# Kernel tuning notes

Hardware: AMD Instinct MI355X
Metric: run time of the kernel (lower is better)

## Reference

```python
import jax, jax.numpy as jnp
import numpy as np

B, G, N_IN, N_HID, N_OUT = 2, 4096, 8, 32, 32
ALPHA, BETA, BN_EPS = 0.005, 5e-5, 1e-5
EDGE_P = 0.05  # adjacency density


def _lin_init(k, fan_in, fan_out):
    k1, k2 = jax.random.split(k)
    lim = 1.0 / np.sqrt(fan_in)
    W = jax.random.uniform(k1, (fan_in, fan_out), minval=-lim, maxval=lim, dtype=jnp.float32)
    b = jax.random.uniform(k2, (fan_out,), minval=-lim, maxval=lim, dtype=jnp.float32)
    return W, b


def setup_inputs() -> dict:
    key = jax.random.key(0)
    ks = jax.random.split(key, 12)
    W_infer, b_infer = _lin_init(ks[0], N_IN, N_HID)
    W_e1, b_e1 = _lin_init(ks[1], 2 * N_HID, 1)
    W_e2, b_e2 = _lin_init(ks[2], 2 * N_HID, 1)
    W_n1, b_n1 = _lin_init(ks[3], 2 * N_HID, N_OUT)
    W_n2, b_n2 = _lin_init(ks[4], 2 * N_HID, N_OUT)
    W_m1, b_m1 = _lin_init(ks[5], 2 * N_HID, N_OUT)
    W_m2, b_m2 = _lin_init(ks[6], 2 * N_HID, N_OUT)
    x = jax.random.normal(ks[7], (B, G, N_IN), dtype=jnp.float32)
    edges1 = jax.random.bernoulli(ks[8], EDGE_P, (G, G)).astype(jnp.float32)
    edges2 = jax.random.bernoulli(ks[9], EDGE_P, (G, G)).astype(jnp.float32)
    bn_gamma = jnp.ones((G,), jnp.float32)
    bn_beta = jnp.zeros((G,), jnp.float32)
    return dict(x=x, edges1=edges1, edges2=edges2, W_infer=W_infer, b_infer=b_infer,
                W_e1=W_e1, b_e1=b_e1, W_e2=W_e2, b_e2=b_e2,
                W_n1=W_n1, b_n1=b_n1, W_n2=W_n2, b_n2=b_n2,
                W_m1=W_m1, b_m1=b_m1, W_m2=W_m2, b_m2=b_m2,
                bn_gamma=bn_gamma, bn_beta=bn_beta)


def _mp_block(x, adj, coef, W_e, b_e, W_n, b_n, W_m, b_m):
    # x: [B,G,H]. Torch builds edge feature at flat index k=i*G+j as cat([x_j, x_i])
    # (shape2 = col gather, shape1 = row gather). We keep the same math without
    # materializing the [B,G*G,2H] tensor.
    Hh = x.shape[-1]
    s_src = x @ W_e[:Hh]   # [B,G,1]  (x_j part of mlp_edge)
    s_dst = x @ W_e[Hh:]   # [B,G,1]  (x_i part of mlp_edge)
    logits = s_dst[:, :, None, 0] + s_src[:, None, :, 0] + b_e[0]   # [B,G,G] at (i,j)
    w = adj + coef * (adj == 0).astype(x.dtype)                     # ori_edge + coef*thres_edge
    e = jax.nn.sigmoid(logits) * w[None]                            # [B,G,G]
    # receive at node i: sum_j e_ij * [x_j, x_i]
    recv_src = jnp.einsum('bij,bjh->bih', e, x)                     # sum_j e_ij x_j
    recv_dst = x * jnp.sum(e, axis=2)[..., None]                    # x_i * sum_j e_ij
    recv = jnp.concatenate([recv_src, recv_dst], axis=-1)           # [B,G,2H]
    recv = jax.nn.elu(recv @ W_n + b_n)                             # nodes_mlp + elu
    upd = jnp.concatenate([recv, x], axis=-1) @ W_m + b_m           # mesg_merge (mode='cat')
    return jax.nn.elu(upd)


def _forward(x, edges1, edges2, W_infer, b_infer, W_e1, b_e1, W_e2, b_e2,
             W_n1, b_n1, W_n2, b_n2, W_m1, b_m1, W_m2, b_m2, bn_gamma, bn_beta):
    h = jax.nn.elu(x @ W_infer + b_infer)                           # infer + elu, [B,G,H]
    h = _mp_block(h, edges1, ALPHA, W_e1, b_e1, W_n1, b_n1, W_m1, b_m1)
    # BatchNorm1d(gene_num) on [B, G, n_out]: per-gene stats over (batch, feature)
    mu = jnp.mean(h, axis=(0, 2), keepdims=True)
    var = jnp.var(h, axis=(0, 2), keepdims=True)
    h = (h - mu) * jax.lax.rsqrt(var + BN_EPS)
    h = h * bn_gamma[None, :, None] + bn_beta[None, :, None]
    return _mp_block(h, edges2, BETA, W_e2, b_e2, W_n2, b_n2, W_m2, b_m2)


def reference(x, edges1, edges2, W_infer, b_infer, W_e1, b_e1, W_e2, b_e2,
              W_n1, b_n1, W_n2, b_n2, W_m1, b_m1, W_m2, b_m2, bn_gamma, bn_beta):
    return _forward(x, edges1, edges2, W_infer, b_infer, W_e1, b_e1, W_e2, b_e2,
                    W_n1, b_n1, W_n2, b_n2, W_m1, b_m1, W_m2, b_m2, bn_gamma, bn_beta)
```

## Files before the change

### kernel.cpp

```cpp
#include <hip/hip_runtime.h>

#define G 4096
#define BSZ 2
#define NIN 8
#define HID 32
#define NLOG2E (-1.4426950408889634f)

typedef __attribute__((ext_vector_type(8))) short short8;
typedef __attribute__((ext_vector_type(4))) float floatx4;
typedef unsigned short ushort_t;
typedef unsigned int uint_t;

__device__ __forceinline__ float elu1(float v) {
    return v > 0.f ? v : (__expf(v) - 1.f);
}
__device__ __forceinline__ ushort_t f2bf(float f) {
    unsigned u = __float_as_uint(f);
    u += 0x7fffu + ((u >> 16) & 1u);
    return (ushort_t)(u >> 16);
}

__global__ __launch_bounds__(256) void k_setup1(
    const float* __restrict__ x, const float* __restrict__ W,
    const float* __restrict__ bias, const float* __restrict__ We,
    float* __restrict__ h0, ushort_t* __restrict__ hTb,
    float* __restrict__ ssrc, float* __restrict__ sdst) {
    __shared__ __align__(16) ushort_t hs[HID][264];
    int tid = threadIdx.x;
    int t = blockIdx.x * 256 + tid;
    int b = t >> 12;
    int g0 = (blockIdx.x & 15) * 256;
    float xin[NIN];
    const float* xp = x + t * NIN;
#pragma unroll
    for (int k = 0; k < NIN; k++) xin[k] = xp[k];
    float ss = 0.f, sd = 0.f;
    float* hp = h0 + (size_t)t * HID;
#pragma unroll
    for (int o = 0; o < HID; o++) {
        float v = bias[o];
#pragma unroll
        for (int k = 0; k < NIN; k++) v += xin[k] * W[k * HID + o];
        v = elu1(v);
        hp[o] = v;
        hs[o][tid] = f2bf(v);
        ss += v * We[o];
        sd += v * We[HID + o];
    }
    ssrc[t] = ss;
    sdst[t] = sd;
    __syncthreads();
#pragma unroll
    for (int p = 0; p < 4; p++) {
        int row = p * 8 + (tid >> 5);
        int c = (tid & 31) * 8;
        short8 v8 = *(const short8*)&hs[row][c];
        *(short8*)(void*)&hTb[(size_t)(b * HID + row) * G + g0 + c] = v8;
    }
}

template <bool DO_BN>
__global__ __launch_bounds__(512, 2) void k_fused(
    const float* __restrict__ adj, const float* __restrict__ ssrc,
    const float* __restrict__ sdst, const ushort_t* __restrict__ hTb_in,
    const float* __restrict__ bep, float coef, const float* __restrict__ hin,
    const float* __restrict__ Wn, const float* __restrict__ bnb,
    const float* __restrict__ Wm, const float* __restrict__ bmb,
    const float* __restrict__ gamma, const float* __restrict__ beta,
    const float* __restrict__ We2, float* __restrict__ outp,
    ushort_t* __restrict__ hTb_out, float* __restrict__ s2s,
    float* __restrict__ s2d) {
    union SMemU {
        float ssm[BSZ][G];
        struct {
            float rec[32][68];
            float rec2[32][68];
            float esg[16][2];
            ushort_t tb[BSZ][HID][16];
        } p;
    };
    __shared__ __align__(16) SMemU sm;
    __shared__ __align__(16) uint_t abits[128][16];
    __shared__ __align__(16) float red[6][64][9];
    __shared__ __align__(16) float Wns[2048];
    __shared__ __align__(16) float Wms[2048];

    int tid = threadIdx.x;
    int g0 = blockIdx.x * 16;
    int l = tid & 63, w = tid >> 6;

    ((float4*)Wns)[tid] = ((const float4*)Wn)[tid];
    ((float4*)Wms)[tid] = ((const float4*)Wm)[tid];
#pragma unroll
    for (int r = 0; r < 4; r++) {
        int idx = r * 2048 + tid * 4;
        int bb = idx >> 12, j = idx & 4095;
        float4 s4 = *(const float4*)&ssrc[bb * G + j];
        s4.x *= NLOG2E; s4.y *= NLOG2E; s4.z *= NLOG2E; s4.w *= NLOG2E;
        *(float4*)&sm.ssm[bb][j] = s4;
    }
#pragma unroll
    for (int rr = 0; rr < 2; rr++) {
        int row = 2 * w + rr;
        const float* ar = adj + (size_t)(g0 + row) * G;
#pragma unroll
        for (int it = 0; it < 16; it++) {
            float4 v4 = *(const float4*)&ar[it * 256 + l * 4];
            uint_t nib = (uint_t)(v4.x != 0.f) | ((uint_t)(v4.y != 0.f) << 1) |
                         ((uint_t)(v4.z != 0.f) << 2) | ((uint_t)(v4.w != 0.f) << 3);
            uint_t wd = nib << ((l & 7) * 4);
            wd |= __shfl_xor(wd, 1);
            wd |= __shfl_xor(wd, 2);
            wd |= __shfl_xor(wd, 4);
            if ((l & 7) == 0) abits[it * 8 + (l >> 3)][row] = wd;
        }
    }

    int jq = w >> 1, b = w & 1;
    int m = l & 15, kg = l >> 4;
    float sd2 = (sdst[b * G + g0 + m] + bep[0]) * NLOG2E;
    float wm1 = 1.f - coef;
    int jstart = jq * 1024;
    const ushort_t* hb0 = hTb_in + (size_t)(b * HID + m) * G + jstart + kg * 8;
    const ushort_t* hb1 = hb0 + (size_t)16 * G;
    floatx4 c0 = {0.f, 0.f, 0.f, 0.f}, c1 = {0.f, 0.f, 0.f, 0.f};
    float es = 0.f;
    short8 pb0[2], pb1[2];
#pragma unroll
    for (int d = 0; d < 2; d++) {
        pb0[d] = *(const short8*)(const void*)(hb0 + d * 32);
        pb1[d] = *(const short8*)(const void*)(hb1 + d * 32);
    }
    __syncthreads();
    const float* svp = &sm.ssm[b][jstart + kg * 8];
    const uint_t* abp = &abits[jq * 32][m];

#pragma unroll 4
    for (int jc = 0; jc < 32; jc++) {
        int cur = jc & 1;
        short8 bf0 = pb0[cur], bf1 = pb1[cur];
        if (jc + 2 < 32) {
            int o = (jc + 2) * 32;
            pb0[cur] = *(const short8*)(const void*)(hb0 + o);
            pb1[cur] = *(const short8*)(const void*)(hb1 + o);
        }
        uint_t bw = abp[jc * 16];
        float4 s0 = *(const float4*)&svp[jc * 32];
        float4 s1 = *(const float4*)&svp[jc * 32 + 4];
        float sv[8] = {s0.x, s0.y, s0.z, s0.w, s1.x, s1.y, s1.z, s1.w};
        short8 af;
#pragma unroll
        for (int t = 0; t < 8; t++) {
            float bitf = (float)((bw >> (kg * 8 + t)) & 1u);
            float wgt = __builtin_fmaf(bitf, wm1, coef);
            float ex = exp2f(sd2 + sv[t]);
            float e = __builtin_amdgcn_rcpf(1.f + ex) * wgt;
            es += e;
            af[t] = (short)f2bf(e);
        }
        c0 = __builtin_amdgcn_mfma_f32_16x16x32_bf16(af, bf0, c0, 0, 0, 0);
        c1 = __builtin_amdgcn_mfma_f32_16x16x32_bf16(af, bf1, c1, 0, 0, 0);
    }
    if (jq) {
        int widx = (jq - 1) * 2 + b;
#pragma unroll
        for (int r = 0; r < 4; r++) {
            red[widx][l][r] = c0[r];
            red[widx][l][4 + r] = c1[r];
        }
        red[widx][l][8] = es;
    }
    __syncthreads();
    if (!jq) {
#pragma unroll
        for (int q = 0; q < 3; q++) {
            int widx = q * 2 + b;
#pragma unroll
            for (int r = 0; r < 4; r++) {
                c0[r] += red[widx][l][r];
                c1[r] += red[widx][l][4 + r];
            }
            es += red[widx][l][8];
        }
        es += __shfl_xor(es, 16);
        es += __shfl_xor(es, 32);
#pragma unroll
        for (int r = 0; r < 4; r++) {
            int gene = (l >> 4) * 4 + r;
            sm.p.rec[gene * 2 + b][m] = c0[r];
            sm.p.rec[gene * 2 + b][16 + m] = c1[r];
        }
        if (l < 16) sm.p.esg[l][b] = es;
    }
    __syncthreads();

    int rl = tid >> 5, hh = tid & 31;
#pragma unroll
    for (int rp = 0; rp < 2; rp++) {
        int row = rp * 16 + rl;
        int gene = row >> 1, bb = row & 1;
        float xv = hin[((size_t)(bb * G + g0 + gene)) * HID + hh];
        sm.p.rec[row][32 + hh] = xv * sm.p.esg[gene][bb];
    }
    __syncthreads();

#pragma unroll
    for (int rp = 0; rp < 2; rp++) {
        int row = rp * 16 + rl;
        int gene = row >> 1, bb = row & 1;
        float v = bnb[hh];
#pragma unroll
        for (int k4 = 0; k4 < 16; k4++) {
            float4 r4 = *(const float4*)&sm.p.rec[row][k4 * 4];
            v += r4.x * Wns[(k4 * 4 + 0) * HID + hh];
            v += r4.y * Wns[(k4 * 4 + 1) * HID + hh];
            v += r4.z * Wns[(k4 * 4 + 2) * HID + hh];
            v += r4.w * Wns[(k4 * 4 + 3) * HID + hh];
        }
        v = elu1(v);
        float xv = hin[((size_t)(bb * G + g0 + gene)) * HID + hh];
        sm.p.rec2[row][hh] = v;
        sm.p.rec2[row][32 + hh] = xv;
        float u = bmb[hh];
#pragma unroll
        for (int k4 = 0; k4 < 16; k4++) {
            float4 r4 = *(const float4*)&sm.p.rec2[row][k4 * 4];
            u += r4.x * Wms[(k4 * 4 + 0) * HID + hh];
            u += r4.y * Wms[(k4 * 4 + 1) * HID + hh];
            u += r4.z * Wms[(k4 * 4 + 2) * HID + hh];
            u += r4.w * Wms[(k4 * 4 + 3) * HID + hh];
        }
        float h1v = elu1(u);
        if (!DO_BN) {
            outp[((size_t)(bb * G + g0 + gene)) * HID + hh] = h1v;
        } else {
            float s = h1v, sq = h1v * h1v;
#pragma unroll
            for (int mm = 32; mm; mm >>= 1) {
                s += __shfl_xor(s, mm);
                sq += __shfl_xor(sq, mm);
            }
            float mu = s * (1.f / 64.f);
            float var = sq * (1.f / 64.f) - mu * mu;
            float rstd = rsqrtf(var + 1e-5f);
            float hn = (h1v - mu) * rstd * gamma[g0 + gene] + beta[g0 + gene];
            outp[((size_t)(bb * G + g0 + gene)) * HID + hh] = hn;
            sm.p.tb[bb][hh][gene] = f2bf(hn);
            float ps = hn * We2[hh], pd = hn * We2[HID + hh];
#pragma unroll
            for (int mm = 16; mm; mm >>= 1) {
                ps += __shfl_xor(ps, mm);
                pd += __shfl_xor(pd, mm);
            }
            if (hh == 0) {
                s2s[bb * G + g0 + gene] = ps;
                s2d[bb * G + g0 + gene] = pd;
            }
        }
    }
    if (DO_BN) {
        __syncthreads();
        if (tid < 128) {
            int b2 = tid >> 6, c = (tid >> 1) & 31, half = tid & 1;
            short8 v8 = *(const short8*)&sm.p.tb[b2][c][half * 8];
            *(short8*)(void*)&hTb_out[(size_t)(b2 * HID + c) * G + g0 + half * 8] = v8;
        }
    }
}

extern "C" void kernel_launch(void* const* d_in, const int* in_sizes, int n_in,
                              void* d_out, int out_size, void* d_ws, size_t ws_size,
                              hipStream_t stream) {
    const float* x      = (const float*)d_in[0];
    const float* edges1 = (const float*)d_in[1];
    const float* edges2 = (const float*)d_in[2];
    const float* W_inf  = (const float*)d_in[3];
    const float* b_inf  = (const float*)d_in[4];
    const float* W_e1   = (const float*)d_in[5];
    const float* b_e1   = (const float*)d_in[6];
    const float* W_e2   = (const float*)d_in[7];
    const float* b_e2   = (const float*)d_in[8];
    const float* W_n1   = (const float*)d_in[9];
    const float* b_n1   = (const float*)d_in[10];
    const float* W_n2   = (const float*)d_in[11];
    const float* b_n2   = (const float*)d_in[12];
    const float* W_m1   = (const float*)d_in[13];
    const float* b_m1   = (const float*)d_in[14];
    const float* W_m2   = (const float*)d_in[15];
    const float* b_m2   = (const float*)d_in[16];
    const float* bn_g   = (const float*)d_in[17];
    const float* bn_b   = (const float*)d_in[18];
    float* out = (float*)d_out;

    float* ws = (float*)d_ws;
    float* h0   = ws;
    float* h1n  = ws + 262144;
    float* s1s  = ws + 524288;
    float* s1d  = ws + 532480;
    float* s2s  = ws + 540672;
    float* s2d  = ws + 548864;
    ushort_t* hTb  = (ushort_t*)(ws + 557056);
    ushort_t* hTb2 = (ushort_t*)(ws + 688128);

    const float ALPHA = 0.005f, BETA = 5e-5f;

    k_setup1<<<32, 256, 0, stream>>>(x, W_inf, b_inf, W_e1, h0, hTb, s1s, s1d);
    k_fused<true><<<G / 16, 512, 0, stream>>>(
        edges1, s1s, s1d, hTb, b_e1, ALPHA, h0, W_n1, b_n1, W_m1, b_m1,
        bn_g, bn_b, W_e2, h1n, hTb2, s2s, s2d);
    k_fused<false><<<G / 16, 512, 0, stream>>>(
        edges2, s2s, s2d, hTb2, b_e2, BETA, h1n, W_n2, b_n2, W_m2, b_m2,
        nullptr, nullptr, nullptr, out, nullptr, nullptr, nullptr);
}
```

Measured before the change: 248.2 us.

## Double the fused-kernel block to 1024 threads and split reduction 8-way

Each fused block now runs 16 waves instead of 8. The column range for each batch is split into eight 512-wide chunks instead of four 1024-wide chunks, so each wave runs half as many MFMA iterations, and the cross-wave reduction buffer grows to match. The adjacency bit-packing is restructured so each thread reads a contiguous slice of every row, and the epilogue MLP/BN covers all 32 rows in a single pass. The intent is more latency hiding and shorter serial loops per CU. The cost is a larger reduction step, more LDS, and a launch-bounds hint that may force a tight register budget and cause spills.

After: 239.8 us. -3.4%, faster.

```diff
diff --git a/kernel.cpp b/kernel.cpp
--- a/kernel.cpp
+++ b/kernel.cpp
@@ -60,7 +60,7 @@
 }
 
 template <bool DO_BN>
-__global__ __launch_bounds__(512, 2) void k_fused(
+__global__ __launch_bounds__(1024, 4) void k_fused(
     const float* __restrict__ adj, const float* __restrict__ ssrc,
     const float* __restrict__ sdst, const ushort_t* __restrict__ hTb_in,
     const float* __restrict__ bep, float coef, const float* __restrict__ hin,
@@ -81,46 +81,50 @@
     };
     __shared__ __align__(16) SMemU sm;
     __shared__ __align__(16) uint_t abits[128][16];
-    __shared__ __align__(16) float red[6][64][9];
+    __shared__ __align__(16) float red[14][64][9];
     __shared__ __align__(16) float Wns[2048];
     __shared__ __align__(16) float Wms[2048];
 
     int tid = threadIdx.x;
     int g0 = blockIdx.x * 16;
     int l = tid & 63, w = tid >> 6;
-
-    ((float4*)Wns)[tid] = ((const float4*)Wn)[tid];
-    ((float4*)Wms)[tid] = ((const float4*)Wm)[tid];
-#pragma unroll
-    for (int r = 0; r < 4; r++) {
-        int idx = r * 2048 + tid * 4;
+    int b = w >> 3, jq = w & 7;
+
+    if (tid < 512) {
+        ((float4*)Wns)[tid] = ((const float4*)Wn)[tid];
+    } else {
+        int t2 = tid - 512;
+        ((float4*)Wms)[t2] = ((const float4*)Wm)[t2];
+    }
+#pragma unroll
+    for (int r = 0; r < 2; r++) {
+        int idx = r * 4096 + tid * 4;
         int bb = idx >> 12, j = idx & 4095;
         float4 s4 = *(const float4*)&ssrc[bb * G + j];
         s4.x *= NLOG2E; s4.y *= NLOG2E; s4.z *= NLOG2E; s4.w *= NLOG2E;
         *(float4*)&sm.ssm[bb][j] = s4;
     }
-#pragma unroll
-    for (int rr = 0; rr < 2; rr++) {
-        int row = 2 * w + rr;
-        const float* ar = adj + (size_t)(g0 + row) * G;
-#pragma unroll
-        for (int it = 0; it < 16; it++) {
-            float4 v4 = *(const float4*)&ar[it * 256 + l * 4];
+    {
+        int jw = tid >> 3;
+        bool st = (tid & 7) == 0;
+        int sh = (tid & 7) * 4;
+#pragma unroll
+        for (int s = 0; s < 16; s++) {
+            float4 v4 = *(const float4*)&adj[(size_t)(g0 + s) * G + tid * 4];
             uint_t nib = (uint_t)(v4.x != 0.f) | ((uint_t)(v4.y != 0.f) << 1) |
                          ((uint_t)(v4.z != 0.f) << 2) | ((uint_t)(v4.w != 0.f) << 3);
-            uint_t wd = nib << ((l & 7) * 4);
+            uint_t wd = nib << sh;
             wd |= __shfl_xor(wd, 1);
             wd |= __shfl_xor(wd, 2);
             wd |= __shfl_xor(wd, 4);
-            if ((l & 7) == 0) abits[it * 8 + (l >> 3)][row] = wd;
-        }
-    }
-
-    int jq = w >> 1, b = w & 1;
+            if (st) abits[jw][s] = wd;
+        }
+    }
+
     int m = l & 15, kg = l >> 4;
     float sd2 = (sdst[b * G + g0 + m] + bep[0]) * NLOG2E;
     float wm1 = 1.f - coef;
-    int jstart = jq * 1024;
+    int jstart = jq * 512;
     const ushort_t* hb0 = hTb_in + (size_t)(b * HID + m) * G + jstart + kg * 8;
     const ushort_t* hb1 = hb0 + (size_t)16 * G;
     floatx4 c0 = {0.f, 0.f, 0.f, 0.f}, c1 = {0.f, 0.f, 0.f, 0.f};
@@ -133,13 +137,13 @@
     }
     __syncthreads();
     const float* svp = &sm.ssm[b][jstart + kg * 8];
-    const uint_t* abp = &abits[jq * 32][m];
+    const uint_t* abp = &abits[jq * 16][m];
 
 #pragma unroll 4
-    for (int jc = 0; jc < 32; jc++) {
+    for (int jc = 0; jc < 16; jc++) {
         int cur = jc & 1;
         short8 bf0 = pb0[cur], bf1 = pb1[cur];
-        if (jc + 2 < 32) {
+        if (jc + 2 < 16) {
             int o = (jc + 2) * 32;
             pb0[cur] = *(const short8*)(const void*)(hb0 + o);
             pb1[cur] = *(const short8*)(const void*)(hb1 + o);
@@ -162,7 +166,7 @@
         c1 = __builtin_amdgcn_mfma_f32_16x16x32_bf16(af, bf1, c1, 0, 0, 0);
     }
     if (jq) {
-        int widx = (jq - 1) * 2 + b;
+        int widx = b * 7 + jq - 1;
 #pragma unroll
         for (int r = 0; r < 4; r++) {
             red[widx][l][r] = c0[r];
@@ -173,8 +177,8 @@
     __syncthreads();
     if (!jq) {
 #pragma unroll
-        for (int q = 0; q < 3; q++) {
-            int widx = q * 2 + b;
+        for (int q = 0; q < 7; q++) {
+            int widx = b * 7 + q;
 #pragma unroll
             for (int r = 0; r < 4; r++) {
                 c0[r] += red[widx][l][r];
@@ -195,70 +199,58 @@
     __syncthreads();
 
     int rl = tid >> 5, hh = tid & 31;
-#pragma unroll
-    for (int rp = 0; rp < 2; rp++) {
-        int row = rp * 16 + rl;
-        int gene = row >> 1, bb = row & 1;
-        float xv = hin[((size_t)(bb * G + g0 + gene)) * HID + hh];
-        sm.p.rec[row][32 + hh] = xv * sm.p.esg[gene][bb];
-    }
-    __syncthreads();
-
-#pragma unroll
-    for (int rp = 0; rp < 2; rp++) {
-        int row = rp * 16 + rl;
-        int gene = row >> 1, bb = row & 1;
-        float v = bnb[hh];
-#pragma unroll
-        for (int k4 = 0; k4 < 16; k4++) {
-            float4 r4 = *(const float4*)&sm.p.rec[row][k4 * 4];
-            v += r4.x * Wns[(k4 * 4 + 0) * HID + hh];
-            v += r4.y * Wns[(k4 * 4 + 1) * HID + hh];
-            v += r4.z * Wns[(k4 * 4 + 2) * HID + hh];
-            v += r4.w * Wns[(k4 * 4 + 3) * HID + hh];
-        }
-        v = elu1(v);
-        float xv = hin[((size_t)(bb * G + g0 + gene)) * HID + hh];
-        sm.p.rec2[row][hh] = v;
-        sm.p.rec2[row][32 + hh] = xv;
-        float u = bmb[hh];
-#pragma unroll
-        for (int k4 = 0; k4 < 16; k4++) {
-            float4 r4 = *(const float4*)&sm.p.rec2[row][k4 * 4];
-            u += r4.x * Wms[(k4 * 4 + 0) * HID + hh];
-            u += r4.y * Wms[(k4 * 4 + 1) * HID + hh];
-            u += r4.z * Wms[(k4 * 4 + 2) * HID + hh];
-            u += r4.w * Wms[(k4 * 4 + 3) * HID + hh];
-        }
-        float h1v = elu1(u);
-        if (!DO_BN) {
-            outp[((size_t)(bb * G + g0 + gene)) * HID + hh] = h1v;
-        } else {
-            float s = h1v, sq = h1v * h1v;
-#pragma unroll
-            for (int mm = 32; mm; mm >>= 1) {
-                s += __shfl_xor(s, mm);
-                sq += __shfl_xor(sq, mm);
-            }
-            float mu = s * (1.f / 64.f);
-            float var = sq * (1.f / 64.f) - mu * mu;
-            float rstd = rsqrtf(var + 1e-5f);
-            float hn = (h1v - mu) * rstd * gamma[g0 + gene] + beta[g0 + gene];
-            outp[((size_t)(bb * G + g0 + gene)) * HID + hh] = hn;
-            sm.p.tb[bb][hh][gene] = f2bf(hn);
-            float ps = hn * We2[hh], pd = hn * We2[HID + hh];
-#pragma unroll
-            for (int mm = 16; mm; mm >>= 1) {
-                ps += __shfl_xor(ps, mm);
-                pd += __shfl_xor(pd, mm);
-            }
-            if (hh == 0) {
-                s2s[bb * G + g0 + gene] = ps;
-                s2d[bb * G + g0 + gene] = pd;
-            }
-        }
-    }
-    if (DO_BN) {
+    int gene = rl >> 1, bb = rl & 1;
+    float xv = hin[((size_t)(bb * G + g0 + gene)) * HID + hh];
+    sm.p.rec[rl][32 + hh] = xv * sm.p.esg[gene][bb];
+    __syncthreads();
+
+    float v = bnb[hh];
+#pragma unroll
+    for (int k4 = 0; k4 < 16; k4++) {
+        float4 r4 = *(const float4*)&sm.p.rec[rl][k4 * 4];
+        v += r4.x * Wns[(k4 * 4 + 0) * HID + hh];
+        v += r4.y * Wns[(k4 * 4 + 1) * HID + hh];
+        v += r4.z * Wns[(k4 * 4 + 2) * HID + hh];
+        v += r4.w * Wns[(k4 * 4 + 3) * HID + hh];
+    }
+    v = elu1(v);
+    sm.p.rec2[rl][hh] = v;
+    sm.p.rec2[rl][32 + hh] = xv;
+    float u = bmb[hh];
+#pragma unroll
+    for (int k4 = 0; k4 < 16; k4++) {
+        float4 r4 = *(const float4*)&sm.p.rec2[rl][k4 * 4];
+        u += r4.x * Wms[(k4 * 4 + 0) * HID + hh];
+        u += r4.y * Wms[(k4 * 4 + 1) * HID + hh];
+        u += r4.z * Wms[(k4 * 4 + 2) * HID + hh];
+        u += r4.w * Wms[(k4 * 4 + 3) * HID + hh];
+    }
+    float h1v = elu1(u);
+    if (!DO_BN) {
+        outp[((size_t)(bb * G + g0 + gene)) * HID + hh] = h1v;
+    } else {
+        float s = h1v, sq = h1v * h1v;
+#pragma unroll
+        for (int mm = 32; mm; mm >>= 1) {
+            s += __shfl_xor(s, mm);
+            sq += __shfl_xor(sq, mm);
+        }
+        float mu = s * (1.f / 64.f);
+        float var = sq * (1.f / 64.f) - mu * mu;
+        float rstd = rsqrtf(var + 1e-5f);
+        float hn = (h1v - mu) * rstd * gamma[g0 + gene] + beta[g0 + gene];
+        outp[((size_t)(bb * G + g0 + gene)) * HID + hh] = hn;
+        sm.p.tb[bb][hh][gene] = f2bf(hn);
+        float ps = hn * We2[hh], pd = hn * We2[HID + hh];
+#pragma unroll
+        for (int mm = 16; mm; mm >>= 1) {
+            ps += __shfl_xor(ps, mm);
+            pd += __shfl_xor(pd, mm);
+        }
+        if (hh == 0) {
+            s2s[bb * G + g0 + gene] = ps;
+            s2d[bb * G + g0 + gene] = pd;
+        }
         __syncthreads();
         if (tid < 128) {
             int b2 = tid >> 6, c = (tid >> 1) & 31, half = tid & 1;
@@ -305,10 +297,10 @@
     const float ALPHA = 0.005f, BETA = 5e-5f;
 
     k_setup1<<<32, 256, 0, stream>>>(x, W_inf, b_inf, W_e1, h0, hTb, s1s, s1d);
-    k_fused<true><<<G / 16, 512, 0, stream>>>(
+    k_fused<true><<<G / 16, 1024, 0, stream>>>(
         edges1, s1s, s1d, hTb, b_e1, ALPHA, h0, W_n1, b_n1, W_m1, b_m1,
         bn_g, bn_b, W_e2, h1n, hTb2, s2s, s2d);
-    k_fused<false><<<G / 16, 512, 0, stream>>>(
+    k_fused<false><<<G / 16, 1024, 0, stream>>>(
         edges2, s2s, s2d, hTb2, b_e2, BETA, h1n, W_n2, b_n2, W_m2, b_m2,
         nullptr, nullptr, nullptr, out, nullptr, nullptr, nullptr);
 }
```
